# Performance work log

Measured on AMD Instinct MI355X. Metric: run time of the kernel, lower is better.

## Reference

```python
import jax, jax.numpy as jnp
import numpy as np

D_OUT = 8192
D_IN = 8192
BA = 64  # block size for A (output side)
BB = 64  # block size for B (input side)
NA = D_OUT // BA
NB = D_IN // BB


def setup_inputs() -> dict:
    key = jax.random.key(0)
    k1, k2, k3 = jax.random.split(key, 3)
    # W plays the role of naive_compression_module.reconstruct(): dense d_out x d_in
    W = jax.random.normal(k1, (D_OUT, D_IN), dtype=jnp.float32)
    # Block-diagonal A (d_out x d_out) stored as stack of diagonal blocks [nA, bA, bA]
    A_blocks = jax.random.normal(k2, (NA, BA, BA), dtype=jnp.float32)
    # Block-diagonal B (d_in x d_in) stored as [nB, bB, bB]
    B_blocks = jax.random.normal(k3, (NB, BB, BB), dtype=jnp.float32)
    return {"W": W, "A_blocks": A_blocks, "B_blocks": B_blocks}


def reference(W, A_blocks, B_blocks):
    # out = A @ W @ B with A, B block-diagonal; skip the zero off-diagonal blocks.
    nA, bA, _ = A_blocks.shape
    nB, bB, _ = B_blocks.shape
    d_out = nA * bA
    d_in = nB * bB
    # Left multiply: each A block acts on its own bA-row slab of W.
    # [nA, bA, bA] @ [nA, bA, d_in] -> [nA, bA, d_in]
    AW = jnp.einsum('nab,nbj->naj', A_blocks, W.reshape(nA, bA, d_in)).reshape(d_out, d_in)
    # Right multiply: each B block acts on its own bB-column slab.
    # [d_out, nB, bB] @ [nB, bB, bB] -> [d_out, nB, bB]
    out = jnp.einsum('inb,nbc->inc', AW.reshape(d_out, nB, bB), B_blocks).reshape(d_out, d_in)
    return out
```

## Files before the change

kernel.cpp:

```cpp
#include <hip/hip_runtime.h>
#include <hip/hip_bf16.h>


#define D 8192
#define BS 64
#define LSTR 72
#define OSTR 68

typedef __bf16  bf16x8 __attribute__((ext_vector_type(8)));
typedef float   f32x4  __attribute__((ext_vector_type(4)));

__device__ __forceinline__ unsigned short f2bf(float f) {
    union { float f; unsigned u; } v; v.f = f;
    unsigned r = v.u + 0x7FFFu + ((v.u >> 16) & 1u);
    return (unsigned short)(r >> 16);
}

__device__ __forceinline__ unsigned pkbf(float lo, float hi) {
    union { __hip_bfloat162 h; unsigned u; } c;
    c.h = __float22bfloat162_rn(make_float2(lo, hi));
    return c.u;
}

__global__ __launch_bounds__(256, 4) void bcl_kernel(
    const float* __restrict__ W,
    const float* __restrict__ Ab,
    const float* __restrict__ Bb,
    float* __restrict__ out)
{
    __shared__ __align__(16) unsigned char smem[36864];
    unsigned short* Wl = (unsigned short*)(smem);
    unsigned short* Al = (unsigned short*)(smem + 9216);
    unsigned short* Bt = (unsigned short*)(smem + 18432);
    unsigned short* Tt = (unsigned short*)(smem + 27648);
    float*          Ol = (float*)(smem);

    const int t = threadIdx.x;
    const int b = blockIdx.x;
    const int a = blockIdx.y;

    const float* Wg = W  + (size_t)a * BS * D + (size_t)b * BS;
    const float* Ag = Ab + (size_t)a * BS * BS;
    const float* Bg = Bb + (size_t)b * BS * BS;

    const int r0 = t >> 4;
    const int c4 = (t & 15) << 2;

    f32x4 w[4], av[4], bv[4];
    #pragma unroll
    for (int i = 0; i < 4; ++i) {
        const int row = i * 16 + r0;
        w[i]  = __builtin_nontemporal_load((const f32x4*)(Wg + (size_t)row * D + c4));
        av[i] = *(const f32x4*)(Ag + row * BS + c4);
        bv[i] = *(const f32x4*)(Bg + row * BS + c4);
    }

    #pragma unroll
    for (int i = 0; i < 4; ++i) {
        const int row = i * 16 + r0;
        uint2 wp;
        wp.x = pkbf(w[i][0], w[i][1]);
        wp.y = pkbf(w[i][2], w[i][3]);
        *(uint2*)&Wl[row * LSTR + c4] = wp;
        Bt[(c4 + 0) * LSTR + row] = f2bf(bv[i][0]);
        Bt[(c4 + 1) * LSTR + row] = f2bf(bv[i][1]);
        Bt[(c4 + 2) * LSTR + row] = f2bf(bv[i][2]);
        Bt[(c4 + 3) * LSTR + row] = f2bf(bv[i][3]);
    }
    __syncthreads();

    const int lane = t & 63;
    const int wv   = t >> 6;
    const int l16  = lane & 15;
    const int quad = lane >> 4;
    const int m0   = wv * 16;

    f32x4 acc[4] = {};
    #pragma unroll
    for (int s = 0; s < 2; ++s) {
        const int k0 = s * 32 + quad * 8;
        bf16x8 af = *(const bf16x8*)&Wl[(m0 + l16) * LSTR + k0];
        #pragma unroll
        for (int j = 0; j < 4; ++j) {
            bf16x8 bf = *(const bf16x8*)&Bt[(j * 16 + l16) * LSTR + k0];
            acc[j] = __builtin_amdgcn_mfma_f32_16x16x32_bf16(af, bf, acc[j], 0, 0, 0);
        }
    }

    #pragma unroll
    for (int i = 0; i < 4; ++i) {
        const int row = i * 16 + r0;
        uint2 ap;
        ap.x = pkbf(av[i][0], av[i][1]);
        ap.y = pkbf(av[i][2], av[i][3]);
        *(uint2*)&Al[row * LSTR + c4] = ap;
    }

    #pragma unroll
    for (int j = 0; j < 4; ++j) {
        uint2 p;
        p.x = pkbf(acc[j][0], acc[j][1]);
        p.y = pkbf(acc[j][2], acc[j][3]);
        *(uint2*)&Tt[(j * 16 + l16) * LSTR + m0 + quad * 4] = p;
    }
    __syncthreads();

    f32x4 acc2[4] = {};
    #pragma unroll
    for (int s = 0; s < 2; ++s) {
        const int k0 = s * 32 + quad * 8;
        bf16x8 af = *(const bf16x8*)&Al[(m0 + l16) * LSTR + k0];
        #pragma unroll
        for (int j = 0; j < 4; ++j) {
            bf16x8 bf = *(const bf16x8*)&Tt[(j * 16 + l16) * LSTR + k0];
            acc2[j] = __builtin_amdgcn_mfma_f32_16x16x32_bf16(af, bf, acc2[j], 0, 0, 0);
        }
    }
    __syncthreads();

    #pragma unroll
    for (int j = 0; j < 4; ++j) {
        #pragma unroll
        for (int r = 0; r < 4; ++r) {
            Ol[(m0 + quad * 4 + r) * OSTR + j * 16 + l16] = acc2[j][r];
        }
    }
    __syncthreads();

    float* Og = out + (size_t)a * BS * D + (size_t)b * BS;
    #pragma unroll
    for (int i = 0; i < 4; ++i) {
        const int row = i * 16 + r0;
        f32x4 v = *(const f32x4*)&Ol[row * OSTR + c4];
        __builtin_nontemporal_store(v, (f32x4*)(Og + (size_t)row * D + c4));
    }
}

extern "C" void kernel_launch(void* const* d_in, const int* in_sizes, int n_in,
                              void* d_out, int out_size, void* d_ws, size_t ws_size,
                              hipStream_t stream) {
    const float* W = (const float*)d_in[0];
    const float* A = (const float*)d_in[1];
    const float* B = (const float*)d_in[2];
    float* o = (float*)d_out;
    dim3 grid(D / BS, D / BS);
    bcl_kernel<<<grid, 256, 0, stream>>>(W, A, B, o);
}
```

Measured before the change: 434.1 us.

## Loop each block over eight A-row tiles with register prefetch and double-buffered LDS

Each workgroup now handles GITER=8 consecutive output row-tiles for one column tile. The B block is converted and held in registers once per workgroup. W and A tiles are loaded straight into MFMA fragment registers, with the next tile prefetched during compute, and the intermediate tile uses a ping-pong LDS buffer so only one barrier is needed per iteration. The output is written straight from accumulators as scalar nontemporal stores instead of being staged through LDS. This cuts block count, B reloads and barriers, but the scalar stores are less coalesced, and the grid has fewer blocks, which reduces parallelism.

```diff
diff --git a/kernel.cpp b/kernel.cpp
--- a/kernel.cpp
+++ b/kernel.cpp
@@ -4,8 +4,8 @@
 
 #define D 8192
 #define BS 64
+#define GITER 8
 #define LSTR 72
-#define OSTR 68
 
 typedef __bf16  bf16x8 __attribute__((ext_vector_type(8)));
 typedef float   f32x4  __attribute__((ext_vector_type(4)));
@@ -22,117 +22,132 @@
     return c.u;
 }
 
+__device__ __forceinline__ bf16x8 mkfrag(f32x4 lo, f32x4 hi) {
+    union { unsigned u[4]; bf16x8 v; } r;
+    r.u[0] = pkbf(lo[0], lo[1]);
+    r.u[1] = pkbf(lo[2], lo[3]);
+    r.u[2] = pkbf(hi[0], hi[1]);
+    r.u[3] = pkbf(hi[2], hi[3]);
+    return r.v;
+}
+
 __global__ __launch_bounds__(256, 4) void bcl_kernel(
     const float* __restrict__ W,
     const float* __restrict__ Ab,
     const float* __restrict__ Bb,
     float* __restrict__ out)
 {
-    __shared__ __align__(16) unsigned char smem[36864];
-    unsigned short* Wl = (unsigned short*)(smem);
-    unsigned short* Al = (unsigned short*)(smem + 9216);
-    unsigned short* Bt = (unsigned short*)(smem + 18432);
-    unsigned short* Tt = (unsigned short*)(smem + 27648);
-    float*          Ol = (float*)(smem);
+    __shared__ __align__(16) unsigned short Bt[BS * LSTR];
+    __shared__ __align__(16) unsigned short Tt[2][BS * LSTR];
 
-    const int t = threadIdx.x;
-    const int b = blockIdx.x;
-    const int a = blockIdx.y;
-
-    const float* Wg = W  + (size_t)a * BS * D + (size_t)b * BS;
-    const float* Ag = Ab + (size_t)a * BS * BS;
-    const float* Bg = Bb + (size_t)b * BS * BS;
-
-    const int r0 = t >> 4;
-    const int c4 = (t & 15) << 2;
-
-    f32x4 w[4], av[4], bv[4];
-    #pragma unroll
-    for (int i = 0; i < 4; ++i) {
-        const int row = i * 16 + r0;
-        w[i]  = __builtin_nontemporal_load((const f32x4*)(Wg + (size_t)row * D + c4));
-        av[i] = *(const f32x4*)(Ag + row * BS + c4);
-        bv[i] = *(const f32x4*)(Bg + row * BS + c4);
-    }
-
-    #pragma unroll
-    for (int i = 0; i < 4; ++i) {
-        const int row = i * 16 + r0;
-        uint2 wp;
-        wp.x = pkbf(w[i][0], w[i][1]);
-        wp.y = pkbf(w[i][2], w[i][3]);
-        *(uint2*)&Wl[row * LSTR + c4] = wp;
-        Bt[(c4 + 0) * LSTR + row] = f2bf(bv[i][0]);
-        Bt[(c4 + 1) * LSTR + row] = f2bf(bv[i][1]);
-        Bt[(c4 + 2) * LSTR + row] = f2bf(bv[i][2]);
-        Bt[(c4 + 3) * LSTR + row] = f2bf(bv[i][3]);
-    }
-    __syncthreads();
+    const int t  = threadIdx.x;
+    const int b  = blockIdx.x;
+    const int a0 = blockIdx.y * GITER;
 
     const int lane = t & 63;
     const int wv   = t >> 6;
     const int l16  = lane & 15;
     const int quad = lane >> 4;
     const int m0   = wv * 16;
+    const int frow = m0 + l16;
+    const int kq   = quad * 8;
 
-    f32x4 acc[4] = {};
-    #pragma unroll
-    for (int s = 0; s < 2; ++s) {
-        const int k0 = s * 32 + quad * 8;
-        bf16x8 af = *(const bf16x8*)&Wl[(m0 + l16) * LSTR + k0];
+    const float* Wp = W   + (size_t)(a0 * BS + frow) * D + b * BS + kq;
+    const float* Ap = Ab  + (size_t)a0 * BS * BS + frow * BS + kq;
+    float*       Op = out + (size_t)(a0 * BS + m0 + quad * 4) * D + b * BS + l16;
+
+    f32x4 w0 = __builtin_nontemporal_load((const f32x4*)(Wp + 0));
+    f32x4 w1 = __builtin_nontemporal_load((const f32x4*)(Wp + 4));
+    f32x4 w2 = __builtin_nontemporal_load((const f32x4*)(Wp + 32));
+    f32x4 w3 = __builtin_nontemporal_load((const f32x4*)(Wp + 36));
+    f32x4 av0 = *(const f32x4*)(Ap + 0);
+    f32x4 av1 = *(const f32x4*)(Ap + 4);
+    f32x4 av2 = *(const f32x4*)(Ap + 32);
+    f32x4 av3 = *(const f32x4*)(Ap + 36);
+
+    {
+        const float* Bg = Bb + (size_t)b * BS * BS;
+        const int r0 = t >> 4;
+        const int c4 = (t & 15) << 2;
         #pragma unroll
-        for (int j = 0; j < 4; ++j) {
-            bf16x8 bf = *(const bf16x8*)&Bt[(j * 16 + l16) * LSTR + k0];
-            acc[j] = __builtin_amdgcn_mfma_f32_16x16x32_bf16(af, bf, acc[j], 0, 0, 0);
-        }
-    }
-
-    #pragma unroll
-    for (int i = 0; i < 4; ++i) {
-        const int row = i * 16 + r0;
-        uint2 ap;
-        ap.x = pkbf(av[i][0], av[i][1]);
-        ap.y = pkbf(av[i][2], av[i][3]);
-        *(uint2*)&Al[row * LSTR + c4] = ap;
-    }
-
-    #pragma unroll
-    for (int j = 0; j < 4; ++j) {
-        uint2 p;
-        p.x = pkbf(acc[j][0], acc[j][1]);
-        p.y = pkbf(acc[j][2], acc[j][3]);
-        *(uint2*)&Tt[(j * 16 + l16) * LSTR + m0 + quad * 4] = p;
-    }
-    __syncthreads();
-
-    f32x4 acc2[4] = {};
-    #pragma unroll
-    for (int s = 0; s < 2; ++s) {
-        const int k0 = s * 32 + quad * 8;
-        bf16x8 af = *(const bf16x8*)&Al[(m0 + l16) * LSTR + k0];
-        #pragma unroll
-        for (int j = 0; j < 4; ++j) {
-            bf16x8 bf = *(const bf16x8*)&Tt[(j * 16 + l16) * LSTR + k0];
-            acc2[j] = __builtin_amdgcn_mfma_f32_16x16x32_bf16(af, bf, acc2[j], 0, 0, 0);
+        for (int i = 0; i < 4; ++i) {
+            const int k = i * 16 + r0;
+            f32x4 v = *(const f32x4*)(Bg + k * BS + c4);
+            Bt[(c4 + 0) * LSTR + k] = f2bf(v[0]);
+            Bt[(c4 + 1) * LSTR + k] = f2bf(v[1]);
+            Bt[(c4 + 2) * LSTR + k] = f2bf(v[2]);
+            Bt[(c4 + 3) * LSTR + k] = f2bf(v[3]);
         }
     }
     __syncthreads();
 
+    bf16x8 btf[4][2];
     #pragma unroll
     for (int j = 0; j < 4; ++j) {
+        btf[j][0] = *(const bf16x8*)&Bt[(j * 16 + l16) * LSTR + kq];
+        btf[j][1] = *(const bf16x8*)&Bt[(j * 16 + l16) * LSTR + 32 + kq];
+    }
+
+    int buf = 0;
+    #pragma unroll 1
+    for (int i = 0; i < GITER; ++i) {
+        bf16x8 waf0 = mkfrag(w0, w1);
+        bf16x8 waf1 = mkfrag(w2, w3);
+        bf16x8 aaf0 = mkfrag(av0, av1);
+        bf16x8 aaf1 = mkfrag(av2, av3);
+
+        if (i + 1 < GITER) {
+            const float* Wn = Wp + (size_t)(i + 1) * BS * D;
+            const float* An = Ap + (i + 1) * BS * BS;
+            w0 = __builtin_nontemporal_load((const f32x4*)(Wn + 0));
+            w1 = __builtin_nontemporal_load((const f32x4*)(Wn + 4));
+            w2 = __builtin_nontemporal_load((const f32x4*)(Wn + 32));
+            w3 = __builtin_nontemporal_load((const f32x4*)(Wn + 36));
+            av0 = *(const f32x4*)(An + 0);
+            av1 = *(const f32x4*)(An + 4);
+            av2 = *(const f32x4*)(An + 32);
+            av3 = *(const f32x4*)(An + 36);
+        }
+
+        f32x4 acc1[4] = {};
         #pragma unroll
-        for (int r = 0; r < 4; ++r) {
-            Ol[(m0 + quad * 4 + r) * OSTR + j * 16 + l16] = acc2[j][r];
+        for (int j = 0; j < 4; ++j)
+            acc1[j] = __builtin_amdgcn_mfma_f32_16x16x32_bf16(waf0, btf[j][0], acc1[j], 0, 0, 0);
+        #pragma unroll
+        for (int j = 0; j < 4; ++j)
+            acc1[j] = __builtin_amdgcn_mfma_f32_16x16x32_bf16(waf1, btf[j][1], acc1[j], 0, 0, 0);
+
+        unsigned short* Tb = Tt[buf];
+        #pragma unroll
+        for (int j = 0; j < 4; ++j) {
+            uint2 p;
+            p.x = pkbf(acc1[j][0], acc1[j][1]);
+            p.y = pkbf(acc1[j][2], acc1[j][3]);
+            *(uint2*)&Tb[(j * 16 + l16) * LSTR + m0 + quad * 4] = p;
         }
-    }
-    __syncthreads();
+        __syncthreads();
 
-    float* Og = out + (size_t)a * BS * D + (size_t)b * BS;
-    #pragma unroll
-    for (int i = 0; i < 4; ++i) {
-        const int row = i * 16 + r0;
-        f32x4 v = *(const f32x4*)&Ol[row * OSTR + c4];
-        __builtin_nontemporal_store(v, (f32x4*)(Og + (size_t)row * D + c4));
+        f32x4 acc2[4] = {};
+        #pragma unroll
+        for (int j = 0; j < 4; ++j) {
+            bf16x8 tf = *(const bf16x8*)&Tb[(j * 16 + l16) * LSTR + kq];
+            acc2[j] = __builtin_amdgcn_mfma_f32_16x16x32_bf16(aaf0, tf, acc2[j], 0, 0, 0);
+        }
+        #pragma unroll
+        for (int j = 0; j < 4; ++j) {
+            bf16x8 tf = *(const bf16x8*)&Tb[(j * 16 + l16) * LSTR + 32 + kq];
+            acc2[j] = __builtin_amdgcn_mfma_f32_16x16x32_bf16(aaf1, tf, acc2[j], 0, 0, 0);
+        }
+
+        float* Or = Op + (size_t)i * BS * D;
+        #pragma unroll
+        for (int j = 0; j < 4; ++j) {
+            #pragma unroll
+            for (int r = 0; r < 4; ++r)
+                __builtin_nontemporal_store(acc2[j][r], Or + (size_t)r * D + j * 16);
+        }
+
+        buf ^= 1;
     }
 }
 
@@ -143,6 +158,6 @@
     const float* A = (const float*)d_in[1];
     const float* B = (const float*)d_in[2];
     float* o = (float*)d_out;
-    dim3 grid(D / BS, D / BS);
+    dim3 grid(D / BS, D / BS / GITER);
     bcl_kernel<<<grid, 256, 0, stream>>>(W, A, B, o);
 }
```

Measured after the change: 463.3 us. +6.7%, slower.
